# Kernel tuning notes

Measured on AMD Instinct MI355X. Metric: run time of the kernel, lower is better.

## Reference

```python
import jax, jax.numpy as jnp
import numpy as np

DIM = 96
HEADS = 4
WS = (2, 7, 7)      # window size (wd, wh, ww)
SS = (1, 3, 3)      # shift size
RES = (16, 56, 56)  # (D, H, W)
BATCH = 4
HIDDEN = 384        # mlp_ratio * dim
EPS = 1e-5


def _rel_pos_index(ws):
    wd, wh, ww = ws
    c = np.stack(np.meshgrid(np.arange(wd), np.arange(wh), np.arange(ww), indexing='ij')).reshape(3, -1)
    r = (c[:, :, None] - c[:, None, :]).transpose(1, 2, 0)  # (N, N, 3)
    r[..., 0] += wd - 1
    r[..., 1] += wh - 1
    r[..., 2] += ww - 1
    r[..., 0] *= (2 * wh - 1) * (2 * ww - 1)
    r[..., 1] *= (2 * ww - 1)
    return r.sum(-1)  # (N, N) int


def _attn_mask(res, ws, ss):
    D, H, W = res
    wd, wh, ww = ws
    sd, sh, sw = ss
    img = np.zeros((D, H, W), np.float32)
    cnt = 0
    for dsl in (slice(0, -wd), slice(-wd, -sd), slice(-sd, None)):
        for hsl in (slice(0, -wh), slice(-wh, -sh), slice(-sh, None)):
            for wsl in (slice(0, -ww), slice(-ww, -sw), slice(-sw, None)):
                img[dsl, hsl, wsl] = cnt
                cnt += 1
    N = wd * wh * ww
    m = img.reshape(D // wd, wd, H // wh, wh, W // ww, ww).transpose(0, 2, 4, 1, 3, 5).reshape(-1, N)
    am = m[:, None, :] - m[:, :, None]
    return np.where(am != 0, np.float32(-100.0), np.float32(0.0))  # (nW, N, N)


def setup_inputs() -> dict:
    key = jax.random.key(0)
    ks = jax.random.split(key, 8)
    s = 0.02
    return {
        'x': jax.random.normal(ks[0], (BATCH, DIM) + RES, jnp.float32),
        'gamma1': jnp.ones((DIM,), jnp.float32),
        'beta1': jnp.zeros((DIM,), jnp.float32),
        'gamma2': jnp.ones((DIM,), jnp.float32),
        'beta2': jnp.zeros((DIM,), jnp.float32),
        'qkv_w': jax.random.normal(ks[1], (DIM, 3 * DIM), jnp.float32) * s,
        'qkv_b': jnp.zeros((3 * DIM,), jnp.float32),
        'proj_w': jax.random.normal(ks[2], (DIM, DIM), jnp.float32) * s,
        'proj_b': jnp.zeros((DIM,), jnp.float32),
        'rpb_table': jax.random.normal(ks[3], ((2 * WS[0] - 1) * (2 * WS[1] - 1) * (2 * WS[2] - 1), HEADS), jnp.float32) * s,
        'fc1_w': jax.random.normal(ks[4], (DIM, HIDDEN), jnp.float32) * s,
        'fc1_b': jnp.zeros((HIDDEN,), jnp.float32),
        'fc2_w': jax.random.normal(ks[5], (HIDDEN, DIM), jnp.float32) * s,
        'fc2_b': jnp.zeros((DIM,), jnp.float32),
    }


def _layernorm(t, g, b):
    mu = t.mean(-1, keepdims=True)
    var = ((t - mu) ** 2).mean(-1, keepdims=True)
    return (t - mu) / jnp.sqrt(var + EPS) * g + b


def reference(x, gamma1, beta1, gamma2, beta2, qkv_w, qkv_b, proj_w, proj_b,
              rpb_table, fc1_w, fc1_b, fc2_w, fc2_b):
    B, C, D, H, W = x.shape
    wd, wh, ww = WS
    sd, sh, sw = SS
    N = wd * wh * ww
    nH = HEADS
    dh = C // nH

    rpi = jnp.asarray(_rel_pos_index(WS))          # (N, N) static
    mask = jnp.asarray(_attn_mask(RES, WS, SS))    # (nW, N, N) static
    nW = mask.shape[0]

    xl = jnp.transpose(x, (0, 2, 3, 4, 1))  # (B, D, H, W, C) channels-last

    # norm1 + cyclic shift
    h = _layernorm(xl, gamma1, beta1)
    h = jnp.roll(h, (-sd, -sh, -sw), axis=(1, 2, 3))

    # window partition -> (B*nW, N, C)
    win = h.reshape(B, D // wd, wd, H // wh, wh, W // ww, ww, C)
    win = win.transpose(0, 1, 3, 5, 2, 4, 6, 7).reshape(-1, N, C)

    # window attention
    qkv = (win @ qkv_w + qkv_b).reshape(-1, N, 3, nH, dh).transpose(2, 0, 3, 1, 4)
    q, k, v = qkv[0] * (dh ** -0.5), qkv[1], qkv[2]  # (B_, nH, N, dh)
    attn = jnp.einsum('bhnd,bhmd->bhnm', q, k)       # (B_, nH, N, N)
    rpb = rpb_table[rpi].transpose(2, 0, 1)          # (nH, N, N)
    attn = attn + rpb[None]
    attn = attn.reshape(B, nW, nH, N, N) + mask[None, :, None]
    attn = jax.nn.softmax(attn.reshape(-1, nH, N, N), axis=-1)
    out = jnp.einsum('bhnm,bhmd->bhnd', attn, v).transpose(0, 2, 1, 3).reshape(-1, N, C)
    out = out @ proj_w + proj_b

    # window reverse + reverse shift
    out = out.reshape(B, D // wd, H // wh, W // ww, wd, wh, ww, C)
    out = out.transpose(0, 1, 4, 2, 5, 3, 6, 7).reshape(B, D, H, W, C)
    out = jnp.roll(out, (sd, sh, sw), axis=(1, 2, 3))

    xl = xl + out  # residual 1

    # norm2 + 1x1-conv FFN (pointwise = matmul over channel)
    h2 = _layernorm(xl, gamma2, beta2)
    h2 = jax.nn.gelu(h2 @ fc1_w + fc1_b, approximate=False) @ fc2_w + fc2_b
    xl = xl + h2  # residual 2

    return jnp.transpose(xl, (0, 4, 1, 2, 3))  # back to (B, C, D, H, W)
```

## Files before the change

kernel.cpp:

```cpp
#include <hip/hip_runtime.h>
#include <hip/hip_bf16.h>
#include <cmath>

#define C_DIM 96
#define RES_D 16
#define RES_H 56
#define RES_W 56
#define BATCH 4
#define SPATIAL (RES_D*RES_H*RES_W)
#define NTOK (BATCH*SPATIAL)
#define NWIN_TOT 2048
#define EPS_LN 1e-5f
#define QSCALE 0.2041241452319315f

#define MPAD 112

#define OFF_P   0
#define OFF_Q   14336
#define OFF_K   28672
#define OFF_VT  43008
#define SM_TOT  59392

typedef float f32x4 __attribute__((ext_vector_type(4)));
typedef short s16x8 __attribute__((ext_vector_type(8)));
typedef unsigned u32x4 __attribute__((ext_vector_type(4)));
typedef unsigned short u16;

__device__ __forceinline__ u16 f2bf(float f) {
    unsigned u = __float_as_uint(f);
    u = (u + 0x7FFF + ((u >> 16) & 1)) >> 16;
    return (u16)u;
}
__device__ __forceinline__ int swzP(int r, int c) {
    return r * 128 + ((((c >> 3) ^ (r & 15)) << 3) | (c & 7));
}
__device__ __forceinline__ int swzQ(int r, int c) {
    return r * 32 + ((((c >> 3) ^ ((r >> 1) & 3)) << 3) | (c & 7));
}

__device__ __forceinline__ float wave_reduce_sum(float v) {
#pragma unroll
    for (int off = 32; off > 0; off >>= 1) v += __shfl_xor(v, off, 64);
    return v;
}

__global__ __launch_bounds__(256) void k_prep(
    const float* __restrict__ qkv_w, const float* __restrict__ proj_w,
    const float* __restrict__ fc1_w, const float* __restrict__ fc2_w,
    const float* __restrict__ rpb_table,
    u16* __restrict__ wq, u16* __restrict__ wp, u16* __restrict__ w1,
    u16* __restrict__ w2, float* __restrict__ rpbm) {
    int i = blockIdx.x * 256 + threadIdx.x;
    if (i < 27648) {
        int j = i / 96, c = i % 96;
        wq[i] = f2bf(qkv_w[c * 288 + j]);
    } else if (i < 36864) {
        int t = i - 27648; int j = t / 96, c = t % 96;
        wp[t] = f2bf(proj_w[c * 96 + j]);
    } else if (i < 73728) {
        int t = i - 36864; int j = t / 96, c = t % 96;
        w1[t] = f2bf(fc1_w[c * 384 + j]);
    } else if (i < 110592) {
        int t = i - 73728; int c = t / 384, j = t % 384;
        w2[t] = f2bf(fc2_w[j * 96 + c]);
    } else if (i < 176128) {
        int t = i - 110592;
        int h = t / 16384, r = t % 16384, n = r / 128, m = r % 128;
        float v;
        if (m >= 98) {
            v = -30000.0f;
        } else if (n >= 98) {
            v = 0.0f;
        } else {
            int dzn = n / 49, rn = n % 49, hyn = rn / 7, wxn = rn % 7;
            int dzm = m / 49, rm = m % 49, hym = rm / 7, wxm = rm % 7;
            int ridx = (dzn - dzm + 1) * 169 + (hyn - hym + 6) * 13 + (wxn - wxm + 6);
            v = rpb_table[ridx * 4 + h];
        }
        rpbm[t] = v;
    }
}

__global__ __launch_bounds__(256) void k_transpose_in(const float* __restrict__ x,
                                                      float* __restrict__ xl) {
    __shared__ float tile[32][33];
    const int b = blockIdx.z;
    const int s0 = blockIdx.x * 32;
    const int c0 = blockIdx.y * 32;
    const float* xb = x + (size_t)b * C_DIM * SPATIAL;
    float* xlb = xl + (size_t)b * SPATIAL * C_DIM;
    const int ts = threadIdx.x, tc = threadIdx.y;
#pragma unroll
    for (int i = 0; i < 32; i += 8)
        tile[tc + i][ts] = xb[(size_t)(c0 + tc + i) * SPATIAL + s0 + ts];
    __syncthreads();
#pragma unroll
    for (int i = 0; i < 32; i += 8)
        xlb[(size_t)(s0 + tc + i) * C_DIM + c0 + ts] = tile[ts][tc + i];
}

__global__ __launch_bounds__(448, 2) void k_win_attn(
    const float* __restrict__ xl, float* __restrict__ xl2,
    const float* __restrict__ g1, const float* __restrict__ b1,
    const u16* __restrict__ wqkv, const float* __restrict__ qkv_b,
    const u16* __restrict__ wproj, const float* __restrict__ proj_b,
    const float* __restrict__ rpbm) {
    __shared__ __align__(16) u16 sm[SM_TOT];
    __shared__ int s_gtok[MPAD];
    __shared__ int s_reg[MPAD];

    const int tid = threadIdx.x;
    const int lane = tid & 63;
    const int wv = tid >> 6;
    const int g4 = lane >> 4;
    const int c16 = lane & 15;
    const int mt = wv;

    const int wid = blockIdx.x;
    const int b = wid >> 9;
    const int rem = wid & 511;
    const int wdi = rem >> 6, whi = (rem >> 3) & 7, wwi = rem & 7;

    for (int i = tid; i < 7168; i += 448) {
        int c = 24 + (i & 7);
        int hb = (i >> 3) / 112;
        int r = (i >> 3) % 112;
        int base = (hb < 4) ? (OFF_Q + hb * 3584) : (OFF_K + (hb - 4) * 3584);
        sm[base + swzQ(r, c)] = 0;
    }
    for (int i = tid; i < 4096; i += 448) {
        int h = i >> 10, rr = 24 + ((i >> 7) & 7), c = i & 127;
        sm[OFF_VT + h * 4096 + swzP(rr, c)] = 0;
    }
    for (int i = tid; i < 1536; i += 448) {
        int h = i / 384, r = (i % 384) >> 4, c = 112 + (i & 15);
        sm[OFF_VT + h * 4096 + swzP(r, c)] = 0;
    }
    for (int i = tid; i < 1792; i += 448) {
        int r = i >> 4, c = 112 + (i & 15);
        sm[OFF_P + swzP(r, c)] = 0;
    }
    if (tid < MPAD) {
        if (tid < 98) {
            const int n = tid;
            const int dz = n / 49, r = n % 49, hy = r / 7, wx = r % 7;
            const int rd = wdi * 2 + dz, rh = whi * 7 + hy, rw = wwi * 7 + wx;
            int od = rd + 1; if (od >= RES_D) od -= RES_D;
            int oh = rh + 3; if (oh >= RES_H) oh -= RES_H;
            int ow = rw + 3; if (ow >= RES_W) ow -= RES_W;
            s_gtok[n] = ((b * RES_D + od) * RES_H + oh) * RES_W + ow;
            const int gd = (rd < 14) ? 0 : (rd < 15 ? 1 : 2);
            const int gh = (rh < 49) ? 0 : (rh < 53 ? 1 : 2);
            const int gw = (rw < 49) ? 0 : (rw < 53 ? 1 : 2);
            s_reg[n] = gd * 9 + gh * 3 + gw;
        } else { s_gtok[tid] = 0; s_reg[tid] = -1; }
    }
    __syncthreads();

    const int myrow = mt * 16 + c16;
    const float live = (myrow < 98) ? 1.0f : 0.0f;
    u32x4 xa[3];
    {
        const float* src = xl + (size_t)s_gtok[myrow] * C_DIM;
        f32x4 xv0 = *(const f32x4*)(src + 0 * 32 + g4 * 8);
        f32x4 xv1 = *(const f32x4*)(src + 0 * 32 + g4 * 8 + 4);
        f32x4 xv2 = *(const f32x4*)(src + 1 * 32 + g4 * 8);
        f32x4 xv3 = *(const f32x4*)(src + 1 * 32 + g4 * 8 + 4);
        f32x4 xv4 = *(const f32x4*)(src + 2 * 32 + g4 * 8);
        f32x4 xv5 = *(const f32x4*)(src + 2 * 32 + g4 * 8 + 4);
        float lsum = (xv0[0]+xv0[1]+xv0[2]+xv0[3]) + (xv1[0]+xv1[1]+xv1[2]+xv1[3])
                   + (xv2[0]+xv2[1]+xv2[2]+xv2[3]) + (xv3[0]+xv3[1]+xv3[2]+xv3[3])
                   + (xv4[0]+xv4[1]+xv4[2]+xv4[3]) + (xv5[0]+xv5[1]+xv5[2]+xv5[3]);
        lsum += __shfl_xor(lsum, 16, 64);
        lsum += __shfl_xor(lsum, 32, 64);
        const float mu = lsum * (1.0f / 96.0f);
        f32x4 d0 = xv0 - mu, d1 = xv1 - mu, d2 = xv2 - mu,
              d3 = xv3 - mu, d4 = xv4 - mu, d5 = xv5 - mu;
        float lvv = (d0[0]*d0[0]+d0[1]*d0[1]+d0[2]*d0[2]+d0[3]*d0[3])
                  + (d1[0]*d1[0]+d1[1]*d1[1]+d1[2]*d1[2]+d1[3]*d1[3])
                  + (d2[0]*d2[0]+d2[1]*d2[1]+d2[2]*d2[2]+d2[3]*d2[3])
                  + (d3[0]*d3[0]+d3[1]*d3[1]+d3[2]*d3[2]+d3[3]*d3[3])
                  + (d4[0]*d4[0]+d4[1]*d4[1]+d4[2]*d4[2]+d4[3]*d4[3])
                  + (d5[0]*d5[0]+d5[1]*d5[1]+d5[2]*d5[2]+d5[3]*d5[3]);
        lvv += __shfl_xor(lvv, 16, 64);
        lvv += __shfl_xor(lvv, 32, 64);
        const float rstd = rsqrtf(lvv * (1.0f / 96.0f) + EPS_LN) * live;
#pragma unroll
        for (int ks = 0; ks < 3; ++ks) {
            const f32x4 ea = (ks == 0) ? d0 : (ks == 1) ? d2 : d4;
            const f32x4 eb = (ks == 0) ? d1 : (ks == 1) ? d3 : d5;
            f32x4 ga = *(const f32x4*)(g1 + ks * 32 + g4 * 8);
            f32x4 gb = *(const f32x4*)(g1 + ks * 32 + g4 * 8 + 4);
            f32x4 ba = *(const f32x4*)(b1 + ks * 32 + g4 * 8);
            f32x4 bb = *(const f32x4*)(b1 + ks * 32 + g4 * 8 + 4);
            f32x4 y0 = ea * rstd * ga + ba * live;
            f32x4 y1 = eb * rstd * gb + bb * live;
            xa[ks][0] = (unsigned)f2bf(y0[0]) | ((unsigned)f2bf(y0[1]) << 16);
            xa[ks][1] = (unsigned)f2bf(y0[2]) | ((unsigned)f2bf(y0[3]) << 16);
            xa[ks][2] = (unsigned)f2bf(y1[0]) | ((unsigned)f2bf(y1[1]) << 16);
            xa[ks][3] = (unsigned)f2bf(y1[2]) | ((unsigned)f2bf(y1[3]) << 16);
        }
    }

#pragma unroll
    for (int sel = 0; sel < 3; ++sel) {
#pragma unroll
        for (int t = 0; t < 6; ++t) {
            const int nt = sel * 6 + t;
            f32x4 acc = {0.f, 0.f, 0.f, 0.f};
#pragma unroll
            for (int ks = 0; ks < 3; ++ks) {
                s16x8 a = __builtin_bit_cast(s16x8, xa[ks]);
                s16x8 bw = *(const s16x8*)(wqkv + (size_t)(nt * 16 + c16) * 96 + ks * 32 + g4 * 8);
                acc = __builtin_amdgcn_mfma_f32_16x16x32_bf16(a, bw, acc, 0, 0, 0);
            }
            const float bias = qkv_b[nt * 16 + c16];
            float v0 = acc[0] + bias, v1 = acc[1] + bias, v2 = acc[2] + bias, v3 = acc[3] + bias;
            if (sel == 0) { v0 *= QSCALE; v1 *= QSCALE; v2 *= QSCALE; v3 *= QSCALE; }
            const int j96 = t * 16 + c16;
            const int h = j96 / 24, d = j96 - h * 24;
            const int row0 = mt * 16 + g4 * 4;
            if (sel == 0) {
                sm[OFF_Q + h * 3584 + swzQ(row0 + 0, d)] = f2bf(v0);
                sm[OFF_Q + h * 3584 + swzQ(row0 + 1, d)] = f2bf(v1);
                sm[OFF_Q + h * 3584 + swzQ(row0 + 2, d)] = f2bf(v2);
                sm[OFF_Q + h * 3584 + swzQ(row0 + 3, d)] = f2bf(v3);
            } else if (sel == 1) {
                sm[OFF_K + h * 3584 + swzQ(row0 + 0, d)] = f2bf(v0);
                sm[OFF_K + h * 3584 + swzQ(row0 + 1, d)] = f2bf(v1);
                sm[OFF_K + h * 3584 + swzQ(row0 + 2, d)] = f2bf(v2);
                sm[OFF_K + h * 3584 + swzQ(row0 + 3, d)] = f2bf(v3);
            } else {
                sm[OFF_VT + h * 4096 + swzP(d, row0 + 0)] = f2bf(v0);
                sm[OFF_VT + h * 4096 + swzP(d, row0 + 1)] = f2bf(v1);
                sm[OFF_VT + h * 4096 + swzP(d, row0 + 2)] = f2bf(v2);
                sm[OFF_VT + h * 4096 + swzP(d, row0 + 3)] = f2bf(v3);
            }
        }
    }
    __syncthreads();

    unsigned ogp[4][2][2];
    const int rbase = mt * 16 + g4 * 4;
    int rgs[4];
#pragma unroll
    for (int r = 0; r < 4; ++r) rgs[r] = s_reg[rbase + r];
#pragma unroll
    for (int h = 0; h < 4; ++h) {
        const s16x8 aq = *(const s16x8*)&sm[OFF_Q + h * 3584 + swzQ(mt * 16 + c16, g4 * 8)];
        const float* rh = rpbm + h * 16384;
        float smr[4] = {0.f, 0.f, 0.f, 0.f};
#pragma unroll
        for (int nt = 0; nt < 7; ++nt) {
            s16x8 bk = *(const s16x8*)&sm[OFF_K + h * 3584 + swzQ(nt * 16 + c16, g4 * 8)];
            f32x4 z = {0.f, 0.f, 0.f, 0.f};
            f32x4 sc = __builtin_amdgcn_mfma_f32_16x16x32_bf16(aq, bk, z, 0, 0, 0);
            const int col = nt * 16 + c16;
            const int creg = s_reg[col];
#pragma unroll
            for (int r = 0; r < 4; ++r) {
                float s = sc[r] + rh[(rbase + r) * 128 + col];
                if (rgs[r] != creg) s -= 100.0f;
                const float e = __expf(s);
                sc[r] = e;
                smr[r] += e;
            }
            sm[OFF_P + swzP(rbase + 0, col)] = f2bf(sc[0]);
            sm[OFF_P + swzP(rbase + 1, col)] = f2bf(sc[1]);
            sm[OFF_P + swzP(rbase + 2, col)] = f2bf(sc[2]);
            sm[OFF_P + swzP(rbase + 3, col)] = f2bf(sc[3]);
        }
#pragma unroll
        for (int r = 0; r < 4; ++r) {
#pragma unroll
            for (int m = 1; m <= 8; m <<= 1) smr[r] += __shfl_xor(smr[r], m, 64);
            smr[r] = 1.0f / fmaxf(smr[r], 1e-30f);
        }
#pragma unroll
        for (int dt = 0; dt < 2; ++dt) {
            f32x4 acc = {0.f, 0.f, 0.f, 0.f};
#pragma unroll
            for (int ks = 0; ks < 4; ++ks) {
                s16x8 ap = *(const s16x8*)&sm[OFF_P + swzP(mt * 16 + c16, ks * 32 + g4 * 8)];
                s16x8 bv = *(const s16x8*)&sm[OFF_VT + h * 4096 + swzP(dt * 16 + c16, ks * 32 + g4 * 8)];
                acc = __builtin_amdgcn_mfma_f32_16x16x32_bf16(ap, bv, acc, 0, 0, 0);
            }
            ogp[h][dt][0] = (unsigned)f2bf(acc[0] * smr[0]) | ((unsigned)f2bf(acc[1] * smr[1]) << 16);
            ogp[h][dt][1] = (unsigned)f2bf(acc[2] * smr[2]) | ((unsigned)f2bf(acc[3] * smr[3]) << 16);
        }
    }

#pragma unroll
    for (int h = 0; h < 4; ++h) {
#pragma unroll
        for (int dt = 0; dt < 2; ++dt) {
            const int d = dt * 16 + c16;
            if (d < 24) {
                const int col = h * 24 + d;
#pragma unroll
                for (int rp = 0; rp < 2; ++rp) {
                    const unsigned u = ogp[h][dt][rp];
                    const int row0 = mt * 16 + g4 * 4 + rp * 2;
                    sm[OFF_P + swzP(row0, col)] = (u16)u;
                    sm[OFF_P + swzP(row0 + 1, col)] = (u16)(u >> 16);
                }
            }
        }
    }

#pragma unroll
    for (int nt = 0; nt < 6; ++nt) {
        f32x4 acc = {0.f, 0.f, 0.f, 0.f};
#pragma unroll
        for (int ks = 0; ks < 3; ++ks) {
            s16x8 a = *(const s16x8*)&sm[OFF_P + swzP(mt * 16 + c16, ks * 32 + g4 * 8)];
            s16x8 bw = *(const s16x8*)(wproj + (size_t)(nt * 16 + c16) * 96 + ks * 32 + g4 * 8);
            acc = __builtin_amdgcn_mfma_f32_16x16x32_bf16(a, bw, acc, 0, 0, 0);
        }
        const int col = nt * 16 + c16;
        const float pb = proj_b[col];
#pragma unroll
        for (int r = 0; r < 4; ++r) {
            const int row = mt * 16 + g4 * 4 + r;
            if (row < 98) {
                const size_t base = (size_t)s_gtok[row] * C_DIM + col;
                xl2[base] = xl[base] + acc[r] + pb;
            }
        }
    }
}

__global__ __launch_bounds__(256) void k_ffn(
    const float* __restrict__ xl2, float* __restrict__ out,
    const float* __restrict__ g2, const float* __restrict__ b2,
    const u16* __restrict__ w1, const float* __restrict__ fc1_b,
    const u16* __restrict__ w2, const float* __restrict__ fc2_b) {
    __shared__ char smem[25088 + 12800];
    u16* s_g = (u16*)smem;
    u16* s_h = (u16*)(smem + 25088);
    float* s_res = (float*)(smem + 25088);

    const int tid = threadIdx.x;
    const int lane = tid & 63;
    const int wave = tid >> 6;
    const int g4 = lane >> 4, c16 = lane & 15;
    const int mt = wave & 1;
    const int nh = wave >> 1;
    const int t0 = blockIdx.x * 32;

    for (int n = wave; n < 32; n += 4) {
        const size_t base = (size_t)(t0 + n) * C_DIM;
        const float v0 = xl2[base + lane];
        const float v1 = (lane < 32) ? xl2[base + 64 + lane] : 0.0f;
        const float mu = wave_reduce_sum(v0 + v1) * (1.0f / 96.0f);
        const float d0 = v0 - mu;
        const float d1 = (lane < 32) ? (v1 - mu) : 0.0f;
        const float var = wave_reduce_sum(d0 * d0 + d1 * d1) * (1.0f / 96.0f);
        const float rstd = rsqrtf(var + EPS_LN);
        s_h[n * 104 + lane] = f2bf(d0 * rstd * g2[lane] + b2[lane]);
        if (lane < 32) s_h[n * 104 + 64 + lane] = f2bf(d1 * rstd * g2[64 + lane] + b2[64 + lane]);
    }
    __syncthreads();

#pragma unroll 1
    for (int i = 0; i < 12; ++i) {
        const int nt = nh * 12 + i;
        f32x4 acc = {0.f, 0.f, 0.f, 0.f};
#pragma unroll
        for (int ks = 0; ks < 3; ++ks) {
            s16x8 a = *(const s16x8*)(&s_h[(mt * 16 + c16) * 104 + ks * 32 + g4 * 8]);
            s16x8 bw = *(const s16x8*)(w1 + (size_t)(nt * 16 + c16) * 96 + ks * 32 + g4 * 8);
            acc = __builtin_amdgcn_mfma_f32_16x16x32_bf16(a, bw, acc, 0, 0, 0);
        }
        const int col = nt * 16 + c16;
        const float bias = fc1_b[col];
#pragma unroll
        for (int r = 0; r < 4; ++r) {
            const float v = acc[r] + bias;
            const float gelu = 0.5f * v * (1.0f + erff(v * 0.70710678118654752f));
            s_g[(mt * 16 + g4 * 4 + r) * 392 + col] = f2bf(gelu);
        }
    }
    __syncthreads();

#pragma unroll 1
    for (int i = 0; i < 3; ++i) {
        const int nt = nh * 3 + i;
        f32x4 acc = {0.f, 0.f, 0.f, 0.f};
#pragma unroll
        for (int ks = 0; ks < 12; ++ks) {
            s16x8 a = *(const s16x8*)(&s_g[(mt * 16 + c16) * 392 + ks * 32 + g4 * 8]);
            s16x8 bw = *(const s16x8*)(w2 + (size_t)(nt * 16 + c16) * 384 + ks * 32 + g4 * 8);
            acc = __builtin_amdgcn_mfma_f32_16x16x32_bf16(a, bw, acc, 0, 0, 0);
        }
        const int col = nt * 16 + c16;
        const float bias = fc2_b[col];
#pragma unroll
        for (int r = 0; r < 4; ++r) {
            const int row = mt * 16 + g4 * 4 + r;
            s_res[row * 100 + col] = acc[r] + bias + xl2[(size_t)(t0 + row) * C_DIM + col];
        }
    }
    __syncthreads();

    const int bb = t0 / SPATIAL;
    const int sbase = t0 % SPATIAL;
    for (int idx = tid; idx < 96 * 32; idx += 256) {
        const int c = idx >> 5, tok = idx & 31;
        out[((size_t)bb * C_DIM + c) * SPATIAL + sbase + tok] = s_res[tok * 100 + c];
    }
}

extern "C" void kernel_launch(void* const* d_in, const int* in_sizes, int n_in,
                              void* d_out, int out_size, void* d_ws, size_t ws_size,
                              hipStream_t stream) {
    const float* x      = (const float*)d_in[0];
    const float* g1     = (const float*)d_in[1];
    const float* be1    = (const float*)d_in[2];
    const float* g2     = (const float*)d_in[3];
    const float* be2    = (const float*)d_in[4];
    const float* qkv_w  = (const float*)d_in[5];
    const float* qkv_b  = (const float*)d_in[6];
    const float* proj_w = (const float*)d_in[7];
    const float* proj_b = (const float*)d_in[8];
    const float* rpb    = (const float*)d_in[9];
    const float* fc1_w  = (const float*)d_in[10];
    const float* fc1_b  = (const float*)d_in[11];
    const float* fc2_w  = (const float*)d_in[12];
    const float* fc2_b  = (const float*)d_in[13];
    float* out = (float*)d_out;

    float* xl  = (float*)d_ws;
    float* xl2 = xl + (size_t)NTOK * C_DIM;
    u16* wq = (u16*)(xl2 + (size_t)NTOK * C_DIM);
    u16* wp = wq + 27648;
    u16* w1 = wp + 9216;
    u16* w2 = w1 + 36864;
    float* rpbm = (float*)(w2 + 36864);

    k_prep<<<688, 256, 0, stream>>>(qkv_w, proj_w, fc1_w, fc2_w, rpb, wq, wp, w1, w2, rpbm);
    k_transpose_in<<<dim3(SPATIAL / 32, C_DIM / 32, BATCH), dim3(32, 8), 0, stream>>>(x, xl);
    k_win_attn<<<NWIN_TOT, 448, 0, stream>>>(xl, xl2, g1, be1, wq, qkv_b, wp, proj_b, rpbm);
    k_ffn<<<NTOK / 32, 256, 0, stream>>>(xl2, out, g2, be2, w1, fc1_b, w2, fc2_b);
}
```

Measured before the change: 427.5 us.

## Keep LayerNorm output in registers and swap MFMA operands in FFN kernel

The FFN kernel now computes LayerNorm2 directly in the registers that feed the MFMA B operand, so the shared-memory staging buffer and one barrier go away. Operands are swapped so the weights form the A side, which lets each lane write packed bf16 GELU outputs and read fc2 results as vector loads. The GELU buffer uses an XOR-swizzled layout to avoid bank conflicts, and a launch_bounds occupancy hint is added. Shared memory per block shrinks, which should allow more resident blocks, but an extra barrier is added before the final residual staging.

```diff
diff --git a/kernel.cpp b/kernel.cpp
--- a/kernel.cpp
+++ b/kernel.cpp
@@ -24,6 +24,7 @@
 typedef float f32x4 __attribute__((ext_vector_type(4)));
 typedef short s16x8 __attribute__((ext_vector_type(8)));
 typedef unsigned u32x4 __attribute__((ext_vector_type(4)));
+typedef unsigned u32x2 __attribute__((ext_vector_type(2)));
 typedef unsigned short u16;
 
 __device__ __forceinline__ u16 f2bf(float f) {
@@ -330,15 +331,13 @@
     }
 }
 
-__global__ __launch_bounds__(256) void k_ffn(
+__global__ __launch_bounds__(256, 6) void k_ffn(
     const float* __restrict__ xl2, float* __restrict__ out,
     const float* __restrict__ g2, const float* __restrict__ b2,
     const u16* __restrict__ w1, const float* __restrict__ fc1_b,
     const u16* __restrict__ w2, const float* __restrict__ fc2_b) {
-    __shared__ char smem[25088 + 12800];
-    u16* s_g = (u16*)smem;
-    u16* s_h = (u16*)(smem + 25088);
-    float* s_res = (float*)(smem + 25088);
+    __shared__ __align__(16) u16 sg[32 * 384];
+    float* s_res = (float*)sg;
 
     const int tid = threadIdx.x;
     const int lane = tid & 63;
@@ -347,20 +346,50 @@
     const int mt = wave & 1;
     const int nh = wave >> 1;
     const int t0 = blockIdx.x * 32;
-
-    for (int n = wave; n < 32; n += 4) {
-        const size_t base = (size_t)(t0 + n) * C_DIM;
-        const float v0 = xl2[base + lane];
-        const float v1 = (lane < 32) ? xl2[base + 64 + lane] : 0.0f;
-        const float mu = wave_reduce_sum(v0 + v1) * (1.0f / 96.0f);
-        const float d0 = v0 - mu;
-        const float d1 = (lane < 32) ? (v1 - mu) : 0.0f;
-        const float var = wave_reduce_sum(d0 * d0 + d1 * d1) * (1.0f / 96.0f);
-        const float rstd = rsqrtf(var + EPS_LN);
-        s_h[n * 104 + lane] = f2bf(d0 * rstd * g2[lane] + b2[lane]);
-        if (lane < 32) s_h[n * 104 + 64 + lane] = f2bf(d1 * rstd * g2[64 + lane] + b2[64 + lane]);
-    }
-    __syncthreads();
+    const int tok = mt * 16 + c16;
+
+    u32x4 xa[3];
+    {
+        const float* src = xl2 + (size_t)(t0 + tok) * C_DIM;
+        f32x4 xv0 = *(const f32x4*)(src + 0 * 32 + g4 * 8);
+        f32x4 xv1 = *(const f32x4*)(src + 0 * 32 + g4 * 8 + 4);
+        f32x4 xv2 = *(const f32x4*)(src + 1 * 32 + g4 * 8);
+        f32x4 xv3 = *(const f32x4*)(src + 1 * 32 + g4 * 8 + 4);
+        f32x4 xv4 = *(const f32x4*)(src + 2 * 32 + g4 * 8);
+        f32x4 xv5 = *(const f32x4*)(src + 2 * 32 + g4 * 8 + 4);
+        float lsum = (xv0[0]+xv0[1]+xv0[2]+xv0[3]) + (xv1[0]+xv1[1]+xv1[2]+xv1[3])
+                   + (xv2[0]+xv2[1]+xv2[2]+xv2[3]) + (xv3[0]+xv3[1]+xv3[2]+xv3[3])
+                   + (xv4[0]+xv4[1]+xv4[2]+xv4[3]) + (xv5[0]+xv5[1]+xv5[2]+xv5[3]);
+        lsum += __shfl_xor(lsum, 16, 64);
+        lsum += __shfl_xor(lsum, 32, 64);
+        const float mu = lsum * (1.0f / 96.0f);
+        f32x4 d0 = xv0 - mu, d1 = xv1 - mu, d2 = xv2 - mu,
+              d3 = xv3 - mu, d4 = xv4 - mu, d5 = xv5 - mu;
+        float lvv = (d0[0]*d0[0]+d0[1]*d0[1]+d0[2]*d0[2]+d0[3]*d0[3])
+                  + (d1[0]*d1[0]+d1[1]*d1[1]+d1[2]*d1[2]+d1[3]*d1[3])
+                  + (d2[0]*d2[0]+d2[1]*d2[1]+d2[2]*d2[2]+d2[3]*d2[3])
+                  + (d3[0]*d3[0]+d3[1]*d3[1]+d3[2]*d3[2]+d3[3]*d3[3])
+                  + (d4[0]*d4[0]+d4[1]*d4[1]+d4[2]*d4[2]+d4[3]*d4[3])
+                  + (d5[0]*d5[0]+d5[1]*d5[1]+d5[2]*d5[2]+d5[3]*d5[3]);
+        lvv += __shfl_xor(lvv, 16, 64);
+        lvv += __shfl_xor(lvv, 32, 64);
+        const float rstd = rsqrtf(lvv * (1.0f / 96.0f) + EPS_LN);
+#pragma unroll
+        for (int ks = 0; ks < 3; ++ks) {
+            const f32x4 ea = (ks == 0) ? d0 : (ks == 1) ? d2 : d4;
+            const f32x4 eb = (ks == 0) ? d1 : (ks == 1) ? d3 : d5;
+            f32x4 ga = *(const f32x4*)(g2 + ks * 32 + g4 * 8);
+            f32x4 gb = *(const f32x4*)(g2 + ks * 32 + g4 * 8 + 4);
+            f32x4 ba = *(const f32x4*)(b2 + ks * 32 + g4 * 8);
+            f32x4 bb = *(const f32x4*)(b2 + ks * 32 + g4 * 8 + 4);
+            f32x4 y0 = ea * rstd * ga + ba;
+            f32x4 y1 = eb * rstd * gb + bb;
+            xa[ks][0] = (unsigned)f2bf(y0[0]) | ((unsigned)f2bf(y0[1]) << 16);
+            xa[ks][1] = (unsigned)f2bf(y0[2]) | ((unsigned)f2bf(y0[3]) << 16);
+            xa[ks][2] = (unsigned)f2bf(y1[0]) | ((unsigned)f2bf(y1[1]) << 16);
+            xa[ks][3] = (unsigned)f2bf(y1[2]) | ((unsigned)f2bf(y1[3]) << 16);
+        }
+    }
 
 #pragma unroll 1
     for (int i = 0; i < 12; ++i) {
@@ -368,46 +397,53 @@
         f32x4 acc = {0.f, 0.f, 0.f, 0.f};
 #pragma unroll
         for (int ks = 0; ks < 3; ++ks) {
-            s16x8 a = *(const s16x8*)(&s_h[(mt * 16 + c16) * 104 + ks * 32 + g4 * 8]);
-            s16x8 bw = *(const s16x8*)(w1 + (size_t)(nt * 16 + c16) * 96 + ks * 32 + g4 * 8);
-            acc = __builtin_amdgcn_mfma_f32_16x16x32_bf16(a, bw, acc, 0, 0, 0);
-        }
-        const int col = nt * 16 + c16;
-        const float bias = fc1_b[col];
+            s16x8 aw = *(const s16x8*)(w1 + (size_t)(nt * 16 + c16) * 96 + ks * 32 + g4 * 8);
+            s16x8 bx = __builtin_bit_cast(s16x8, xa[ks]);
+            acc = __builtin_amdgcn_mfma_f32_16x16x32_bf16(aw, bx, acc, 0, 0, 0);
+        }
+        const f32x4 bias = *(const f32x4*)(fc1_b + nt * 16 + g4 * 4);
+        float gv[4];
 #pragma unroll
         for (int r = 0; r < 4; ++r) {
-            const float v = acc[r] + bias;
-            const float gelu = 0.5f * v * (1.0f + erff(v * 0.70710678118654752f));
-            s_g[(mt * 16 + g4 * 4 + r) * 392 + col] = f2bf(gelu);
-        }
-    }
-    __syncthreads();
-
+            const float v = acc[r] + bias[r];
+            gv[r] = 0.5f * v * (1.0f + erff(v * 0.70710678118654752f));
+        }
+        const unsigned lo = (unsigned)f2bf(gv[0]) | ((unsigned)f2bf(gv[1]) << 16);
+        const unsigned hi = (unsigned)f2bf(gv[2]) | ((unsigned)f2bf(gv[3]) << 16);
+        const int chunk = (2 * nt + (g4 >> 1)) ^ (tok & 15);
+        u32x2 pk = {lo, hi};
+        *(u32x2*)&sg[tok * 384 + chunk * 8 + (g4 & 1) * 4] = pk;
+    }
+    __syncthreads();
+
+    f32x4 facc[3];
 #pragma unroll 1
     for (int i = 0; i < 3; ++i) {
         const int nt = nh * 3 + i;
         f32x4 acc = {0.f, 0.f, 0.f, 0.f};
 #pragma unroll
         for (int ks = 0; ks < 12; ++ks) {
-            s16x8 a = *(const s16x8*)(&s_g[(mt * 16 + c16) * 392 + ks * 32 + g4 * 8]);
-            s16x8 bw = *(const s16x8*)(w2 + (size_t)(nt * 16 + c16) * 384 + ks * 32 + g4 * 8);
-            acc = __builtin_amdgcn_mfma_f32_16x16x32_bf16(a, bw, acc, 0, 0, 0);
-        }
-        const int col = nt * 16 + c16;
-        const float bias = fc2_b[col];
-#pragma unroll
-        for (int r = 0; r < 4; ++r) {
-            const int row = mt * 16 + g4 * 4 + r;
-            s_res[row * 100 + col] = acc[r] + bias + xl2[(size_t)(t0 + row) * C_DIM + col];
-        }
+            s16x8 aw = *(const s16x8*)(w2 + (size_t)(nt * 16 + c16) * 384 + ks * 32 + g4 * 8);
+            s16x8 bg = *(const s16x8*)&sg[tok * 384 + (((ks * 4 + g4) ^ (tok & 15)) << 3)];
+            acc = __builtin_amdgcn_mfma_f32_16x16x32_bf16(aw, bg, acc, 0, 0, 0);
+        }
+        const f32x4 bias = *(const f32x4*)(fc2_b + nt * 16 + g4 * 4);
+        const f32x4 res = *(const f32x4*)(xl2 + (size_t)(t0 + tok) * C_DIM + nt * 16 + g4 * 4);
+        facc[i] = acc + bias + res;
+    }
+    __syncthreads();
+#pragma unroll
+    for (int i = 0; i < 3; ++i) {
+        const int nt = nh * 3 + i;
+        *(f32x4*)&s_res[tok * 100 + nt * 16 + g4 * 4] = facc[i];
     }
     __syncthreads();
 
     const int bb = t0 / SPATIAL;
     const int sbase = t0 % SPATIAL;
     for (int idx = tid; idx < 96 * 32; idx += 256) {
-        const int c = idx >> 5, tok = idx & 31;
-        out[((size_t)bb * C_DIM + c) * SPATIAL + sbase + tok] = s_res[tok * 100 + c];
+        const int c = idx >> 5, tk = idx & 31;
+        out[((size_t)bb * C_DIM + c) * SPATIAL + sbase + tk] = s_res[tk * 100 + c];
     }
 }
 
```

Result: slower. 442.9 us (+3.6%).
